# Performance work log

Hardware: AMD Instinct MI355X
Metric: run time of the kernel (lower is better)

Reference implementation:

```python
import jax, jax.numpy as jnp
import numpy as np

B, S, C = 16, 720, 862      # batch, seq_len, enc_in
P = 24                      # highest_freq_period
PAD = 720                   # seq_len % P == 0 -> pad_len == seq_len (no padding branch taken)
LQ = PAD // P               # 30, per-branch subsequence length == conv channels
DM = 128                    # d_model (PECBlock hidden conv channels)
EL = 2                      # e_layers
PRED = 336                  # pred_len
EPS = 1e-5                  # RevIN eps


def setup_inputs() -> dict:
    key = jax.random.key(0)
    ks = jax.random.split(key, 6)
    x = jax.random.normal(ks[0], (B, S, C), jnp.float32)
    # per-layer, per-branch pointwise conv weights (kernel_size=1, no bias)
    W1 = jax.random.normal(ks[1], (EL, P, DM, LQ), jnp.float32) * 0.05   # conv1: LQ -> DM
    W2 = jax.random.normal(ks[2], (EL, P, LQ, DM), jnp.float32) * 0.05   # conv2: DM -> LQ
    proj_w = jax.random.normal(ks[3], (PRED, S), jnp.float32) * 0.02      # Linear(seq_len, pred_len)
    proj_b = jnp.zeros((PRED,), jnp.float32)
    rev_w = jnp.ones((C,), jnp.float32)    # RevIN affine weight
    rev_b = jnp.zeros((C,), jnp.float32)   # RevIN affine bias
    return dict(x=x, W1=W1, W2=W2, proj_w=proj_w, proj_b=proj_b, rev_w=rev_w, rev_b=rev_b)


def reference(x, W1, W2, proj_w, proj_b, rev_w, rev_b):
    # RevIN 'norm': stats over time dim (unbiased=False var), affine
    mean = jnp.mean(x, axis=1, keepdims=True)
    stdev = jnp.sqrt(jnp.var(x, axis=1, keepdims=True) + EPS)
    xn = (x - mean) / stdev * rev_w + rev_b

    # seq_len % P == 0 so pad_time_series is identity
    x_padded = xn
    # NOTE: original loop feeds x_padded into EVERY block (not chained),
    # so each iteration overwrites y; replicated faithfully.
    # Strided gather idx::P == reshape (B,C,LQ,P) and index last axis;
    # scatter reassembly y[:,:,idx::P]=... == reshape back from (B,C,LQ,P).
    xs = x_padded.transpose(0, 2, 1).reshape(B, C, LQ, P)  # (B,C,LQ,P)
    y = x_padded
    for l in range(EL):
        h = jax.nn.gelu(jnp.einsum('pdq,bcqp->pbdc', W1[l], xs), approximate=False)  # (P,B,DM,C)
        ys = jnp.einsum('pqd,pbdc->bcqp', W2[l], h)                                  # (B,C,LQ,P)
        y = ys.reshape(B, C, PAD).transpose(0, 2, 1)                                 # (B,PAD,C)

    # PredictedProjection: Linear over time dim
    out = jnp.einsum('ps,bsc->bpc', proj_w, y[:, :S, :]) + proj_b[None, :, None]  # (B,PRED,C)

    # RevIN 'denorm'
    out = (out - rev_b) / (rev_w + EPS * EPS)
    out = out * stdev + mean
    return out
```

## Files before the change

kernel.cpp:

```cpp
#include <hip/hip_runtime.h>
#include <math.h>

typedef __attribute__((ext_vector_type(8))) short bf16x8;
typedef __attribute__((ext_vector_type(4))) short short4v;
typedef __attribute__((ext_vector_type(4))) float f32x4;

#define NB 16
#define NS 720
#define NC 862
#define NP 24
#define NQ 30
#define NDM 128
#define NPRED 336
#define BC (NB*NC)
#define SCH 10
#define SLEN 72
#define KP 768
#define PBASE (4*BC)
#define WOFF_F (24*BC)
#define NCOL (NB*NC)

__device__ __forceinline__ short f2bf(float f) {
    union { float f; unsigned u; } v; v.f = f;
    unsigned r = v.u + 0x7FFFu + ((v.u >> 16) & 1u);
    return (short)(r >> 16);
}

__device__ __forceinline__ unsigned cvt_pk_bf16(float a, float b) {
    unsigned r;
    asm("v_cvt_pk_bf16_f32 %0, %1, %2" : "=v"(r) : "v"(a), "v"(b));
    return r;
}

__device__ __forceinline__ float gelu_f(float h) {
    float z2 = h * h;
    float zz = h * (0.79788456f + 0.035677408f * z2);
    float e  = __expf(-2.f * zz);
    return h * __builtin_amdgcn_rcpf(1.f + e);
}

__device__ __forceinline__ void gl_lds16(const void* g, void* l) {
    __builtin_amdgcn_global_load_lds(
        (const __attribute__((address_space(1))) unsigned int*)g,
        (__attribute__((address_space(3))) unsigned int*)l, 16, 0, 0);
}

__global__ __launch_bounds__(256) void stats_partial_k(const float* __restrict__ x,
                                                       float* __restrict__ ws) {
    int b = blockIdx.x, half = blockIdx.y, ch = blockIdx.z;
    int t = half * 256 + threadIdx.x;
    if (t >= NC / 2) return;
    const float2* xp = (const float2*)(x + ((size_t)b * NS + (size_t)ch * SLEN) * NC) + t;
    float2 s = {0.f, 0.f}, sq = {0.f, 0.f};
    #pragma unroll 4
    for (int i = 0; i < SLEN; ++i) {
        float2 v = xp[(size_t)i * (NC / 2)];
        s.x += v.x; s.y += v.y;
        sq.x += v.x * v.x; sq.y += v.y * v.y;
    }
    int idx = b * NC + t * 2;
    float* ps = ws + PBASE;
    *(float2*)&ps[(size_t)ch * BC + idx] = s;
    *(float2*)&ps[(size_t)(SCH + ch) * BC + idx] = sq;
}

__global__ __launch_bounds__(256) void stats_final_k(float* __restrict__ ws,
                                                     const float* __restrict__ revw,
                                                     const float* __restrict__ revb) {
    int idx = blockIdx.x * 256 + threadIdx.x;
    if (idx >= BC) return;
    const float* ps = ws + PBASE;
    float s = 0.f, sq = 0.f;
    #pragma unroll
    for (int ch = 0; ch < SCH; ++ch) {
        s  += ps[(size_t)ch * BC + idx];
        sq += ps[(size_t)(SCH + ch) * BC + idx];
    }
    int c = idx % NC;
    float mean  = s * (1.f / NS);
    float var   = sq * (1.f / NS) - mean * mean;
    float stdev = sqrtf(var + 1e-5f);
    float rstd  = 1.f / stdev;
    float aw = revw[c] * rstd;
    float u  = stdev / (revw[c] + 1e-10f);
    ws[idx]          = aw;
    ws[BC + idx]     = revb[c] - mean * aw;
    ws[2 * BC + idx] = u;
    ws[3 * BC + idx] = mean - revb[c] * u;
}

__global__ __launch_bounds__(256) void wprep_k(const float* __restrict__ W1,
                                               const float* __restrict__ W2,
                                               unsigned short* __restrict__ W1FF,
                                               unsigned short* __restrict__ W2FF) {
    int p = blockIdx.x, tid = threadIdx.x;
    const float* w1 = W1 + (size_t)(NP + p) * NDM * NQ;
    const float* w2 = W2 + (size_t)(NP + p) * NQ * NDM;
    #pragma unroll
    for (int pass = 0; pass < 2; ++pass) {
        int s = pass * 256 + tid;
        int l = s & 63, lr = l & 15, lg = l >> 4;
        {
            int dt = s >> 6;
            int d = dt * 16 + lr;
            bf16x8 v;
            #pragma unroll
            for (int j = 0; j < 8; ++j) {
                int q = 8 * lg + j;
                v[j] = f2bf(q < NQ ? w1[d * NQ + q] : 0.f);
            }
            ((bf16x8*)(W1FF + (size_t)p * 4096))[s] = v;
        }
        {
            int g = s >> 6, mi = g >> 2, ks = g & 3;
            int q = mi * 16 + lr, k = ks * 32 + 8 * lg;
            bf16x8 v;
            #pragma unroll
            for (int j = 0; j < 8; ++j)
                v[j] = f2bf(q < NQ ? w2[q * NDM + k + j] : 0.f);
            ((bf16x8*)(W2FF + (size_t)p * 4096))[s] = v;
        }
    }
}

__global__ __launch_bounds__(256) void pwprep_k(const float* __restrict__ pw,
                                                unsigned short* __restrict__ PWPF) {
    int t = blockIdx.x * 256 + threadIdx.x;
    if (t >= 24 * 24 * 64) return;
    int l = t & 63, ks = (t >> 6) % 24, st = t / (24 * 64);
    int lr = l & 15, lg = l >> 4;
    int m = st * 16 + lr;
    bf16x8 v;
    #pragma unroll
    for (int j = 0; j < 8; ++j) {
        int q = 8 * lg + j;
        v[j] = f2bf((m < NPRED && q < NQ) ? pw[(size_t)m * NS + q * NP + ks] : 0.f);
    }
    ((bf16x8*)PWPF)[t] = v;
}

__global__ __launch_bounds__(512, 4) void branch_k(const float* __restrict__ x,
        const unsigned short* __restrict__ W1FF, const unsigned short* __restrict__ W2FF,
        const float* __restrict__ ws, unsigned short* __restrict__ y_t) {
    __shared__ __align__(16) short XsB[4 * 128 * 8];
    __shared__ __align__(16) short HB [16 * 128 * 8];
    int tid = threadIdx.x;
    int c0 = blockIdx.x * 128;
    int p  = blockIdx.y;
    int b  = blockIdx.z;

    {
        int cS = tid & 127, kbS = tid >> 7;
        int cgS = c0 + cS;
        bool cv = cgS < NC;
        int ce = cv ? cgS : NC - 1;
        float aw = ws[b * NC + ce];
        float bw = ws[BC + b * NC + ce];
        const float* xb = x + ((size_t)b * NS + p) * NC + ce;
        float xs[8];
        #pragma unroll
        for (int j = 0; j < 8; ++j) {
            int q = kbS * 8 + j;
            xs[j] = (q < NQ && cv) ? xb[(size_t)q * NP * NC] * aw + bw : 0.f;
        }
        unsigned u[4];
        #pragma unroll
        for (int i = 0; i < 4; ++i) u[i] = cvt_pk_bf16(xs[2 * i], xs[2 * i + 1]);
        *(uint4*)&XsB[(size_t)(kbS * 128 + (cS ^ kbS)) * 8] = *(uint4*)u;
    }

    int w = tid >> 6, l = tid & 63, lr = l & 15, lg = l >> 4;
    f32x4 zf = {0.f, 0.f, 0.f, 0.f};
    const bf16x8* w1p = (const bf16x8*)(W1FF + (size_t)p * 4096);
    const bf16x8* w2p = (const bf16x8*)(W2FF + (size_t)p * 4096);
    bf16x8 a0 = w1p[w * 64 + l];
    bf16x8 w2f[8];
    #pragma unroll
    for (int g = 0; g < 8; ++g) w2f[g] = w2p[g * 64 + l];

    __syncthreads();

    f32x4 hc[8];
    #pragma unroll
    for (int ni = 0; ni < 8; ++ni) {
        bf16x8 bfr = *(const bf16x8*)&XsB[(size_t)(lg * 128 + ((ni * 16 + lr) ^ lg)) * 8];
        hc[ni] = __builtin_amdgcn_mfma_f32_16x16x32_bf16(a0, bfr, zf, 0, 0, 0);
    }
    {
        int d0 = w * 16 + 4 * lg;
        int kb = d0 >> 3, sub = d0 & 7;
        #pragma unroll
        for (int ni = 0; ni < 8; ++ni) {
            unsigned u0 = cvt_pk_bf16(gelu_f(hc[ni][0]), gelu_f(hc[ni][1]));
            unsigned u1 = cvt_pk_bf16(gelu_f(hc[ni][2]), gelu_f(hc[ni][3]));
            int col = ni * 16 + lr;
            unsigned* dst = (unsigned*)&HB[(size_t)(kb * 128 + (col ^ kb)) * 8 + sub];
            dst[0] = u0; dst[1] = u1;
        }
    }
    __syncthreads();

    f32x4 yacc[2] = {zf, zf};
    #pragma unroll
    for (int ks = 0; ks < 4; ++ks) {
        int kb = ks * 4 + lg;
        bf16x8 hfr = *(const bf16x8*)&HB[(size_t)(kb * 128 + ((w * 16 + lr) ^ kb)) * 8];
        #pragma unroll
        for (int mi = 0; mi < 2; ++mi)
            yacc[mi] = __builtin_amdgcn_mfma_f32_16x16x32_bf16(w2f[mi * 4 + ks], hfr,
                                                              yacc[mi], 0, 0, 0);
    }
    int cg2 = c0 + w * 16 + lr;
    if (cg2 < NC) {
        unsigned short* base = y_t + ((size_t)(b * NC + cg2)) * KP + p * 32;
        #pragma unroll
        for (int mi = 0; mi < 2; ++mi) {
            int q0 = mi * 16 + 4 * lg;
            unsigned u0 = cvt_pk_bf16(yacc[mi][0], yacc[mi][1]);
            unsigned u1 = (q0 + 2 < NQ) ? cvt_pk_bf16(yacc[mi][2], yacc[mi][3]) : 0u;
            uint2 uv = make_uint2(u0, u1);
            *(uint2*)(base + q0) = uv;
        }
    }
}

__global__ __launch_bounds__(256, 4) void proj_k(const unsigned short* __restrict__ PWPF,
        const float* __restrict__ pb, const float* __restrict__ ws,
        const unsigned short* __restrict__ y_t, float* __restrict__ out) {
    __shared__ __align__(16) short L[2][12 * 512];
    int tid = threadIdx.x;
    int w = tid >> 6, l = tid & 63, lr = l & 15, lg = l >> 4;
    int gn0 = blockIdx.x * 128;
    int m0  = blockIdx.y * 64;
    f32x4 zf = {0.f, 0.f, 0.f, 0.f};
    f32x4 acc[4][2];
    #pragma unroll
    for (int mi = 0; mi < 4; ++mi) { acc[mi][0] = zf; acc[mi][1] = zf; }

    int cgA = gn0 + (2 * w) * 16 + lr;      if (cgA > NCOL - 1) cgA = NCOL - 1;
    int cgB = gn0 + (2 * w + 1) * 16 + lr;  if (cgB > NCOL - 1) cgB = NCOL - 1;
    const unsigned short* bsrcA = y_t + (size_t)cgA * KP + lg * 8;
    const unsigned short* bsrcB = y_t + (size_t)cgB * KP + lg * 8;
    const unsigned short* asrc  = PWPF + ((size_t)(m0 / 16 + w) * 24) * 512 + (size_t)l * 8;

#define STAGE(BUF, KS) do {                                              \
        gl_lds16(asrc  + (size_t)(KS) * 512, &L[BUF][w * 512]);          \
        gl_lds16(bsrcA + (size_t)(KS) * 32,  &L[BUF][(4 + 2 * w) * 512]);\
        gl_lds16(bsrcB + (size_t)(KS) * 32,  &L[BUF][(5 + 2 * w) * 512]);\
    } while (0)

    STAGE(0, 0);
    __syncthreads();
    int cur = 0;
    for (int ks = 0; ks < 24; ++ks) {
        if (ks + 1 < 24) STAGE(cur ^ 1, ks + 1);
        const short* Lc = L[cur];
        bf16x8 b0 = *(const bf16x8*)&Lc[(4 + 2 * w) * 512 + l * 8];
        bf16x8 b1 = *(const bf16x8*)&Lc[(5 + 2 * w) * 512 + l * 8];
        #pragma unroll
        for (int mi = 0; mi < 4; ++mi) {
            bf16x8 a = *(const bf16x8*)&Lc[mi * 512 + l * 8];
            acc[mi][0] = __builtin_amdgcn_mfma_f32_16x16x32_bf16(a, b0, acc[mi][0], 0, 0, 0);
            acc[mi][1] = __builtin_amdgcn_mfma_f32_16x16x32_bf16(a, b1, acc[mi][1], 0, 0, 0);
        }
        __syncthreads();
        cur ^= 1;
    }
#undef STAGE

    #pragma unroll
    for (int mi = 0; mi < 4; ++mi) {
        #pragma unroll
        for (int r = 0; r < 4; ++r) {
            int pr = m0 + mi * 16 + 4 * lg + r;
            if (pr >= NPRED) continue;
            float bias = pb[pr];
            #pragma unroll
            for (int nj = 0; nj < 2; ++nj) {
                int cg = gn0 + (2 * w + nj) * 16 + lr;
                if (cg >= NCOL) continue;
                int bb = cg / NC;
                int cc = cg - bb * NC;
                out[((size_t)bb * NPRED + pr) * NC + cc] =
                    (acc[mi][nj][r] + bias) * ws[2 * BC + cg] + ws[3 * BC + cg];
            }
        }
    }
}

extern "C" void kernel_launch(void* const* d_in, const int* in_sizes, int n_in,
                              void* d_out, int out_size, void* d_ws, size_t ws_size,
                              hipStream_t stream) {
    const float* x   = (const float*)d_in[0];
    const float* W1  = (const float*)d_in[1];
    const float* W2  = (const float*)d_in[2];
    const float* pw  = (const float*)d_in[3];
    const float* pb  = (const float*)d_in[4];
    const float* rw  = (const float*)d_in[5];
    const float* rb  = (const float*)d_in[6];
    float* out = (float*)d_out;
    float* ws  = (float*)d_ws;
    unsigned short* W1FF = (unsigned short*)(ws + WOFF_F);
    unsigned short* W2FF = W1FF + NP * 4096;
    unsigned short* PWPF = W2FF + NP * 4096;
    unsigned short* y_t  = PWPF + 24 * 24 * 64 * 8;

    stats_partial_k<<<dim3(NB, 2, SCH), 256, 0, stream>>>(x, ws);
    wprep_k<<<dim3(NP), 256, 0, stream>>>(W1, W2, W1FF, W2FF);
    pwprep_k<<<dim3((24 * 24 * 64 + 255) / 256), 256, 0, stream>>>(pw, PWPF);
    stats_final_k<<<dim3((BC + 255) / 256), 256, 0, stream>>>(ws, rw, rb);
    branch_k<<<dim3(7, NP, NB), 512, 0, stream>>>(x, W1FF, W2FF, ws, y_t);
    proj_k<<<dim3((NCOL + 127) / 128, 6), 256, 0, stream>>>(PWPF, pb, ws, y_t, out);
}
```

Before: 85.61 us.

## Fold W2 into projection weights and fuse branch and projection GEMMs

Precomputes G = proj_w · W2 per branch (a weight-only product), so the second conv and the time projection collapse into one GEMM from the GELU hidden state straight to the output. The separate branch and projection kernels become one kernel that loops over the 24 branches per 64-column tile and accumulates the output in registers. This removes the bf16 y_t intermediate round-trip through global memory and one launch. The cost is a 128-wide contraction per branch instead of 30, which adds MFMA work, and only about 216 blocks of 512 threads are launched.

```diff
diff --git a/kernel.cpp b/kernel.cpp
--- a/kernel.cpp
+++ b/kernel.cpp
@@ -2,7 +2,6 @@
 #include <math.h>
 
 typedef __attribute__((ext_vector_type(8))) short bf16x8;
-typedef __attribute__((ext_vector_type(4))) short short4v;
 typedef __attribute__((ext_vector_type(4))) float f32x4;
 
 #define NB 16
@@ -15,10 +14,10 @@
 #define BC (NB*NC)
 #define SCH 10
 #define SLEN 72
-#define KP 768
 #define PBASE (4*BC)
 #define WOFF_F (24*BC)
 #define NCOL (NB*NC)
+#define MT 24
 
 __device__ __forceinline__ short f2bf(float f) {
     union { float f; unsigned u; } v; v.f = f;
@@ -37,12 +36,6 @@
     float zz = h * (0.79788456f + 0.035677408f * z2);
     float e  = __expf(-2.f * zz);
     return h * __builtin_amdgcn_rcpf(1.f + e);
-}
-
-__device__ __forceinline__ void gl_lds16(const void* g, void* l) {
-    __builtin_amdgcn_global_load_lds(
-        (const __attribute__((address_space(1))) unsigned int*)g,
-        (__attribute__((address_space(3))) unsigned int*)l, 16, 0, 0);
 }
 
 __global__ __launch_bounds__(256) void stats_partial_k(const float* __restrict__ x,
@@ -89,200 +82,152 @@
     ws[3 * BC + idx] = mean - revb[c] * u;
 }
 
-__global__ __launch_bounds__(256) void wprep_k(const float* __restrict__ W1,
-                                               const float* __restrict__ W2,
-                                               unsigned short* __restrict__ W1FF,
-                                               unsigned short* __restrict__ W2FF) {
+__global__ __launch_bounds__(256) void w1prep_k(const float* __restrict__ W1,
+                                                unsigned short* __restrict__ W1FF) {
     int p = blockIdx.x, tid = threadIdx.x;
     const float* w1 = W1 + (size_t)(NP + p) * NDM * NQ;
-    const float* w2 = W2 + (size_t)(NP + p) * NQ * NDM;
     #pragma unroll
     for (int pass = 0; pass < 2; ++pass) {
         int s = pass * 256 + tid;
         int l = s & 63, lr = l & 15, lg = l >> 4;
-        {
-            int dt = s >> 6;
-            int d = dt * 16 + lr;
-            bf16x8 v;
-            #pragma unroll
-            for (int j = 0; j < 8; ++j) {
-                int q = 8 * lg + j;
-                v[j] = f2bf(q < NQ ? w1[d * NQ + q] : 0.f);
-            }
-            ((bf16x8*)(W1FF + (size_t)p * 4096))[s] = v;
-        }
-        {
-            int g = s >> 6, mi = g >> 2, ks = g & 3;
-            int q = mi * 16 + lr, k = ks * 32 + 8 * lg;
-            bf16x8 v;
-            #pragma unroll
-            for (int j = 0; j < 8; ++j)
-                v[j] = f2bf(q < NQ ? w2[q * NDM + k + j] : 0.f);
-            ((bf16x8*)(W2FF + (size_t)p * 4096))[s] = v;
-        }
-    }
-}
-
-__global__ __launch_bounds__(256) void pwprep_k(const float* __restrict__ pw,
-                                                unsigned short* __restrict__ PWPF) {
-    int t = blockIdx.x * 256 + threadIdx.x;
-    if (t >= 24 * 24 * 64) return;
-    int l = t & 63, ks = (t >> 6) % 24, st = t / (24 * 64);
-    int lr = l & 15, lg = l >> 4;
-    int m = st * 16 + lr;
+        int dt = s >> 6;
+        int d = dt * 16 + lr;
+        bf16x8 v;
+        #pragma unroll
+        for (int j = 0; j < 8; ++j) {
+            int q = 8 * lg + j;
+            v[j] = f2bf(q < NQ ? w1[d * NQ + q] : 0.f);
+        }
+        ((bf16x8*)(W1FF + (size_t)p * 4096))[s] = v;
+    }
+}
+
+__global__ __launch_bounds__(256) void gprep_k(const float* __restrict__ pw,
+                                               const float* __restrict__ W2,
+                                               unsigned short* __restrict__ GF) {
+    __shared__ float pws[16][NQ + 2];
+    int p = blockIdx.x, mt = blockIdx.y, tid = threadIdx.x;
+    if (tid < 240) {
+        #pragma unroll
+        for (int k = 0; k < 2; ++k) {
+            int idx = tid + k * 240;
+            int mi = idx / NQ, q = idx % NQ;
+            int m = mt * 16 + mi;
+            pws[mi][q] = (m < NPRED) ? pw[(size_t)m * NS + q * NP + p] : 0.f;
+        }
+    }
+    __syncthreads();
+    int ks = tid >> 6, l = tid & 63, lr = l & 15, lg = l >> 4;
+    const float* w2 = W2 + (size_t)(NP + p) * NQ * NDM + ks * 32 + lg * 8;
+    float g[8] = {0, 0, 0, 0, 0, 0, 0, 0};
+    for (int q = 0; q < NQ; ++q) {
+        float pv = pws[lr][q];
+        #pragma unroll
+        for (int j = 0; j < 8; ++j) g[j] += pv * w2[q * NDM + j];
+    }
     bf16x8 v;
     #pragma unroll
-    for (int j = 0; j < 8; ++j) {
-        int q = 8 * lg + j;
-        v[j] = f2bf((m < NPRED && q < NQ) ? pw[(size_t)m * NS + q * NP + ks] : 0.f);
-    }
-    ((bf16x8*)PWPF)[t] = v;
-}
-
-__global__ __launch_bounds__(512, 4) void branch_k(const float* __restrict__ x,
-        const unsigned short* __restrict__ W1FF, const unsigned short* __restrict__ W2FF,
-        const float* __restrict__ ws, unsigned short* __restrict__ y_t) {
-    __shared__ __align__(16) short XsB[4 * 128 * 8];
-    __shared__ __align__(16) short HB [16 * 128 * 8];
+    for (int j = 0; j < 8; ++j) v[j] = f2bf(g[j]);
+    ((bf16x8*)GF)[((size_t)(p * MT + mt) * 4 + ks) * 64 + l] = v;
+}
+
+__global__ __launch_bounds__(512, 2) void mega_k(const float* __restrict__ x,
+        const unsigned short* __restrict__ W1FF, const unsigned short* __restrict__ GF,
+        const float* __restrict__ pb, const float* __restrict__ ws,
+        float* __restrict__ out) {
+    __shared__ __align__(16) short XsB[4 * 64 * 8];
+    __shared__ __align__(16) short HB [16 * 64 * 8];
     int tid = threadIdx.x;
-    int c0 = blockIdx.x * 128;
-    int p  = blockIdx.y;
-    int b  = blockIdx.z;
-
-    {
-        int cS = tid & 127, kbS = tid >> 7;
-        int cgS = c0 + cS;
-        bool cv = cgS < NC;
-        int ce = cv ? cgS : NC - 1;
-        float aw = ws[b * NC + ce];
-        float bw = ws[BC + b * NC + ce];
-        const float* xb = x + ((size_t)b * NS + p) * NC + ce;
-        float xs[8];
-        #pragma unroll
-        for (int j = 0; j < 8; ++j) {
-            int q = kbS * 8 + j;
-            xs[j] = (q < NQ && cv) ? xb[(size_t)q * NP * NC] * aw + bw : 0.f;
-        }
-        unsigned u[4];
-        #pragma unroll
-        for (int i = 0; i < 4; ++i) u[i] = cvt_pk_bf16(xs[2 * i], xs[2 * i + 1]);
-        *(uint4*)&XsB[(size_t)(kbS * 128 + (cS ^ kbS)) * 8] = *(uint4*)u;
-    }
-
+    int n0 = blockIdx.x * 64;
     int w = tid >> 6, l = tid & 63, lr = l & 15, lg = l >> 4;
     f32x4 zf = {0.f, 0.f, 0.f, 0.f};
-    const bf16x8* w1p = (const bf16x8*)(W1FF + (size_t)p * 4096);
-    const bf16x8* w2p = (const bf16x8*)(W2FF + (size_t)p * 4096);
-    bf16x8 a0 = w1p[w * 64 + l];
-    bf16x8 w2f[8];
-    #pragma unroll
-    for (int g = 0; g < 8; ++g) w2f[g] = w2p[g * 64 + l];
-
-    __syncthreads();
-
-    f32x4 hc[8];
-    #pragma unroll
-    for (int ni = 0; ni < 8; ++ni) {
-        bf16x8 bfr = *(const bf16x8*)&XsB[(size_t)(lg * 128 + ((ni * 16 + lr) ^ lg)) * 8];
-        hc[ni] = __builtin_amdgcn_mfma_f32_16x16x32_bf16(a0, bfr, zf, 0, 0, 0);
-    }
-    {
-        int d0 = w * 16 + 4 * lg;
-        int kb = d0 >> 3, sub = d0 & 7;
-        #pragma unroll
-        for (int ni = 0; ni < 8; ++ni) {
-            unsigned u0 = cvt_pk_bf16(gelu_f(hc[ni][0]), gelu_f(hc[ni][1]));
-            unsigned u1 = cvt_pk_bf16(gelu_f(hc[ni][2]), gelu_f(hc[ni][3]));
-            int col = ni * 16 + lr;
-            unsigned* dst = (unsigned*)&HB[(size_t)(kb * 128 + (col ^ kb)) * 8 + sub];
-            dst[0] = u0; dst[1] = u1;
-        }
-    }
-    __syncthreads();
-
-    f32x4 yacc[2] = {zf, zf};
-    #pragma unroll
-    for (int ks = 0; ks < 4; ++ks) {
-        int kb = ks * 4 + lg;
-        bf16x8 hfr = *(const bf16x8*)&HB[(size_t)(kb * 128 + ((w * 16 + lr) ^ kb)) * 8];
-        #pragma unroll
-        for (int mi = 0; mi < 2; ++mi)
-            yacc[mi] = __builtin_amdgcn_mfma_f32_16x16x32_bf16(w2f[mi * 4 + ks], hfr,
-                                                              yacc[mi], 0, 0, 0);
-    }
-    int cg2 = c0 + w * 16 + lr;
-    if (cg2 < NC) {
-        unsigned short* base = y_t + ((size_t)(b * NC + cg2)) * KP + p * 32;
-        #pragma unroll
-        for (int mi = 0; mi < 2; ++mi) {
-            int q0 = mi * 16 + 4 * lg;
-            unsigned u0 = cvt_pk_bf16(yacc[mi][0], yacc[mi][1]);
-            unsigned u1 = (q0 + 2 < NQ) ? cvt_pk_bf16(yacc[mi][2], yacc[mi][3]) : 0u;
-            uint2 uv = make_uint2(u0, u1);
-            *(uint2*)(base + q0) = uv;
-        }
-    }
-}
-
-__global__ __launch_bounds__(256, 4) void proj_k(const unsigned short* __restrict__ PWPF,
-        const float* __restrict__ pb, const float* __restrict__ ws,
-        const unsigned short* __restrict__ y_t, float* __restrict__ out) {
-    __shared__ __align__(16) short L[2][12 * 512];
-    int tid = threadIdx.x;
-    int w = tid >> 6, l = tid & 63, lr = l & 15, lg = l >> 4;
-    int gn0 = blockIdx.x * 128;
-    int m0  = blockIdx.y * 64;
-    f32x4 zf = {0.f, 0.f, 0.f, 0.f};
-    f32x4 acc[4][2];
-    #pragma unroll
-    for (int mi = 0; mi < 4; ++mi) { acc[mi][0] = zf; acc[mi][1] = zf; }
-
-    int cgA = gn0 + (2 * w) * 16 + lr;      if (cgA > NCOL - 1) cgA = NCOL - 1;
-    int cgB = gn0 + (2 * w + 1) * 16 + lr;  if (cgB > NCOL - 1) cgB = NCOL - 1;
-    const unsigned short* bsrcA = y_t + (size_t)cgA * KP + lg * 8;
-    const unsigned short* bsrcB = y_t + (size_t)cgB * KP + lg * 8;
-    const unsigned short* asrc  = PWPF + ((size_t)(m0 / 16 + w) * 24) * 512 + (size_t)l * 8;
-
-#define STAGE(BUF, KS) do {                                              \
-        gl_lds16(asrc  + (size_t)(KS) * 512, &L[BUF][w * 512]);          \
-        gl_lds16(bsrcA + (size_t)(KS) * 32,  &L[BUF][(4 + 2 * w) * 512]);\
-        gl_lds16(bsrcB + (size_t)(KS) * 32,  &L[BUF][(5 + 2 * w) * 512]);\
-    } while (0)
-
-    STAGE(0, 0);
-    __syncthreads();
-    int cur = 0;
-    for (int ks = 0; ks < 24; ++ks) {
-        if (ks + 1 < 24) STAGE(cur ^ 1, ks + 1);
-        const short* Lc = L[cur];
-        bf16x8 b0 = *(const bf16x8*)&Lc[(4 + 2 * w) * 512 + l * 8];
-        bf16x8 b1 = *(const bf16x8*)&Lc[(5 + 2 * w) * 512 + l * 8];
-        #pragma unroll
-        for (int mi = 0; mi < 4; ++mi) {
-            bf16x8 a = *(const bf16x8*)&Lc[mi * 512 + l * 8];
-            acc[mi][0] = __builtin_amdgcn_mfma_f32_16x16x32_bf16(a, b0, acc[mi][0], 0, 0, 0);
-            acc[mi][1] = __builtin_amdgcn_mfma_f32_16x16x32_bf16(a, b1, acc[mi][1], 0, 0, 0);
+    f32x4 acc[3][4];
+    #pragma unroll
+    for (int t = 0; t < 3; ++t)
+        #pragma unroll
+        for (int nt = 0; nt < 4; ++nt) acc[t][nt] = zf;
+
+    int cS = tid & 63, kbS = (tid >> 6) & 3;
+    int n_s = n0 + cS; if (n_s > NCOL - 1) n_s = NCOL - 1;
+    float aw = ws[n_s];
+    float bw = ws[BC + n_s];
+    int b_s = n_s / NC, c_s = n_s - b_s * NC;
+    const float* xb = x + (size_t)b_s * NS * NC + c_s;
+
+    for (int p = 0; p < NP; ++p) {
+        if (tid < 256) {
+            float xs[8];
+            #pragma unroll
+            for (int j = 0; j < 8; ++j) {
+                int q = kbS * 8 + j;
+                xs[j] = (q < NQ) ? xb[(size_t)(q * NP + p) * NC] * aw + bw : 0.f;
+            }
+            unsigned u[4];
+            #pragma unroll
+            for (int i = 0; i < 4; ++i) u[i] = cvt_pk_bf16(xs[2 * i], xs[2 * i + 1]);
+            *(uint4*)&XsB[(size_t)(kbS * 64 + (cS ^ kbS)) * 8] = *(uint4*)u;
         }
         __syncthreads();
-        cur ^= 1;
-    }
-#undef STAGE
-
-    #pragma unroll
-    for (int mi = 0; mi < 4; ++mi) {
+
+        const bf16x8* w1p = (const bf16x8*)(W1FF + (size_t)p * 4096);
+        bf16x8 a0 = w1p[w * 64 + l];
+        f32x4 hc[4];
+        #pragma unroll
+        for (int nt = 0; nt < 4; ++nt) {
+            bf16x8 bfr = *(const bf16x8*)&XsB[(size_t)(lg * 64 + ((nt * 16 + lr) ^ lg)) * 8];
+            hc[nt] = __builtin_amdgcn_mfma_f32_16x16x32_bf16(a0, bfr, zf, 0, 0, 0);
+        }
+        {
+            int d0 = w * 16 + 4 * lg;
+            int kb = d0 >> 3, sub = d0 & 7;
+            #pragma unroll
+            for (int nt = 0; nt < 4; ++nt) {
+                unsigned u0 = cvt_pk_bf16(gelu_f(hc[nt][0]), gelu_f(hc[nt][1]));
+                unsigned u1 = cvt_pk_bf16(gelu_f(hc[nt][2]), gelu_f(hc[nt][3]));
+                int col = nt * 16 + lr;
+                unsigned* dst = (unsigned*)&HB[(size_t)(kb * 64 + (col ^ kb)) * 8 + sub];
+                dst[0] = u0; dst[1] = u1;
+            }
+        }
+        __syncthreads();
+
+        const bf16x8* gp = (const bf16x8*)GF + (size_t)p * MT * 4 * 64 + l;
+        #pragma unroll
+        for (int ks = 0; ks < 4; ++ks) {
+            bf16x8 bfr[4];
+            #pragma unroll
+            for (int nt = 0; nt < 4; ++nt) {
+                int kb = ks * 4 + lg;
+                bfr[nt] = *(const bf16x8*)&HB[(size_t)(kb * 64 + ((nt * 16 + lr) ^ kb)) * 8];
+            }
+            #pragma unroll
+            for (int t = 0; t < 3; ++t) {
+                int mt = w + 8 * t;
+                bf16x8 a = gp[(size_t)(mt * 4 + ks) * 64];
+                #pragma unroll
+                for (int nt = 0; nt < 4; ++nt)
+                    acc[t][nt] = __builtin_amdgcn_mfma_f32_16x16x32_bf16(a, bfr[nt],
+                                                                        acc[t][nt], 0, 0, 0);
+            }
+        }
+    }
+
+    #pragma unroll
+    for (int t = 0; t < 3; ++t) {
+        int mt = w + 8 * t;
         #pragma unroll
         for (int r = 0; r < 4; ++r) {
-            int pr = m0 + mi * 16 + 4 * lg + r;
+            int pr = mt * 16 + 4 * lg + r;
             if (pr >= NPRED) continue;
             float bias = pb[pr];
             #pragma unroll
-            for (int nj = 0; nj < 2; ++nj) {
-                int cg = gn0 + (2 * w + nj) * 16 + lr;
-                if (cg >= NCOL) continue;
-                int bb = cg / NC;
-                int cc = cg - bb * NC;
+            for (int nt = 0; nt < 4; ++nt) {
+                int n = n0 + nt * 16 + lr;
+                if (n >= NCOL) continue;
+                int bb = n / NC;
+                int cc = n - bb * NC;
                 out[((size_t)bb * NPRED + pr) * NC + cc] =
-                    (acc[mi][nj][r] + bias) * ws[2 * BC + cg] + ws[3 * BC + cg];
+                    (acc[t][nt][r] + bias) * ws[2 * BC + n] + ws[3 * BC + n];
             }
         }
     }
@@ -301,14 +246,11 @@
     float* out = (float*)d_out;
     float* ws  = (float*)d_ws;
     unsigned short* W1FF = (unsigned short*)(ws + WOFF_F);
-    unsigned short* W2FF = W1FF + NP * 4096;
-    unsigned short* PWPF = W2FF + NP * 4096;
-    unsigned short* y_t  = PWPF + 24 * 24 * 64 * 8;
+    unsigned short* GF   = W1FF + NP * 4096;
 
     stats_partial_k<<<dim3(NB, 2, SCH), 256, 0, stream>>>(x, ws);
-    wprep_k<<<dim3(NP), 256, 0, stream>>>(W1, W2, W1FF, W2FF);
-    pwprep_k<<<dim3((24 * 24 * 64 + 255) / 256), 256, 0, stream>>>(pw, PWPF);
+    w1prep_k<<<dim3(NP), 256, 0, stream>>>(W1, W1FF);
+    gprep_k<<<dim3(NP, MT), 256, 0, stream>>>(pw, W2, GF);
     stats_final_k<<<dim3((BC + 255) / 256), 256, 0, stream>>>(ws, rw, rb);
-    branch_k<<<dim3(7, NP, NB), 512, 0, stream>>>(x, W1FF, W2FF, ws, y_t);
-    proj_k<<<dim3((NCOL + 127) / 128, 6), 256, 0, stream>>>(PWPF, pb, ws, y_t, out);
-}
+    mega_k<<<dim3((NCOL + 63) / 64), 512, 0, stream>>>(x, W1FF, GF, pb, ws, out);
+}
```

Measured after the change: 190.4 us. 122% more time.
